# Optimization experiments

Measured on AMD Instinct MI355X. Metric: run time of the kernel, lower is better.

## Reference

```python
import jax, jax.numpy as jnp
import numpy as np

V = 32000  # vocab size
H = 128    # embedding dim
B = 16     # batch
S = 256    # seq len

def setup_inputs() -> dict:
    key = jax.random.key(0)
    k1, k2, k3 = jax.random.split(key, 3)
    src = jax.random.randint(k1, (B, S), 0, V, dtype=jnp.int64)
    W = jax.random.normal(k2, (H, V), dtype=jnp.float32) * 0.02  # nn.Linear(v, h).weight: [h, v]
    b = jax.random.normal(k3, (H,), dtype=jnp.float32) * 0.02    # nn.Linear bias: [h]
    return {"src": src, "W": W, "b": b}

def reference(src, W, b):
    # Original: one-hot(src) [B,S,V] @ W.T [V,H] + b  (disguised embedding gather).
    onehot = jax.nn.one_hot(src, V, dtype=W.dtype)          # [B, S, V]
    out = jnp.einsum('bsv,hv->bsh', onehot, W) + b          # [B, S, H]
    return out
```

## Files before the change

kernel.cpp:

```cpp
#include <hip/hip_runtime.h>
#include <hip/hip_bf16.h>


#define VOCAB  32000
#define HDIM   128
#define NTOK   (16 * 256)
#define VPB    32
#define NBLK   (VOCAB / VPB)
#define STRIDE 33

__global__ __launch_bounds__(256) void embed_scatter_kernel(
    const int* __restrict__ src,
    const float* __restrict__ W,
    const float* __restrict__ bias,
    float* __restrict__ out)
{
    __shared__ float tile[HDIM * STRIDE];
    __shared__ int   list[NTOK];
    __shared__ int   nmatch;

    const int t  = threadIdx.x;
    const int v0 = blockIdx.x * VPB;

    if (t == 0) nmatch = 0;
    __syncthreads();

    {
        const int c4 = t & 7;
        const int h0 = t >> 3;
        for (int h = h0; h < HDIM; h += 32) {
            const float4 v = *(const float4*)(W + (size_t)h * VOCAB + v0 + c4 * 4);
            float* dst = &tile[h * STRIDE + c4 * 4];
            dst[0] = v.x; dst[1] = v.y; dst[2] = v.z; dst[3] = v.w;
        }
    }

    {
        const int4* src4 = (const int4*)src;
        for (int i = t; i < NTOK / 4; i += 256) {
            const int4 s = src4[i];
            const int base = i << 2;
            unsigned d;
            d = (unsigned)(s.x - v0); if (d < VPB) list[atomicAdd(&nmatch, 1)] = ((base + 0) << 5) | (int)d;
            d = (unsigned)(s.y - v0); if (d < VPB) list[atomicAdd(&nmatch, 1)] = ((base + 1) << 5) | (int)d;
            d = (unsigned)(s.z - v0); if (d < VPB) list[atomicAdd(&nmatch, 1)] = ((base + 2) << 5) | (int)d;
            d = (unsigned)(s.w - v0); if (d < VPB) list[atomicAdd(&nmatch, 1)] = ((base + 3) << 5) | (int)d;
        }
    }
    __syncthreads();

    const int    n      = nmatch;
    const int    lane32 = t & 31;
    const int    h0     = lane32 * 4;
    const float4 bb     = ((const float4*)bias)[lane32];
    for (int j = t >> 5; j < n; j += 8) {
        const int e   = list[j];
        const int tok = e >> 5;
        const int col = e & 31;
        float4 r;
        r.x = tile[(h0 + 0) * STRIDE + col] + bb.x;
        r.y = tile[(h0 + 1) * STRIDE + col] + bb.y;
        r.z = tile[(h0 + 2) * STRIDE + col] + bb.z;
        r.w = tile[(h0 + 3) * STRIDE + col] + bb.w;
        *(float4*)(out + (size_t)tok * HDIM + h0) = r;
    }
}

extern "C" void kernel_launch(void* const* d_in, const int* in_sizes, int n_in,
                              void* d_out, int out_size, void* d_ws, size_t ws_size,
                              hipStream_t stream) {
    const int*   src  = (const int*)d_in[0];
    const float* W    = (const float*)d_in[1];
    const float* bias = (const float*)d_in[2];
    float*       out  = (float*)d_out;

    embed_scatter_kernel<<<NBLK, 256, 0, stream>>>(src, W, bias, out);
}
```

Baseline: 9.874 us.

## Replace shared atomics with per-wave ballot compaction and overlap loads

Drops the shared-memory atomicAdd counter used to build the match list. Each 64-lane wave now compacts its matches with ballot/popcount into its own list segment. All src and W loads are issued up front into registers before the shared stores, so global latency overlaps and one barrier is removed. The output phase walks the four per-wave lists with one 64-lane wave per token row writing float2, in place of half-waves writing float4. The cost is more registers per thread and a different store width.

```diff
diff --git a/kernel.cpp b/kernel.cpp
--- a/kernel.cpp
+++ b/kernel.cpp
@@ -17,52 +17,69 @@
 {
     __shared__ float tile[HDIM * STRIDE];
     __shared__ int   list[NTOK];
-    __shared__ int   nmatch;
+    __shared__ int   counts[4];
 
-    const int t  = threadIdx.x;
-    const int v0 = blockIdx.x * VPB;
+    const int t    = threadIdx.x;
+    const int lane = t & 63;
+    const int wav  = t >> 6;
+    const int v0   = blockIdx.x * VPB;
 
-    if (t == 0) nmatch = 0;
+    const int4* src4 = (const int4*)src;
+    int4 sv[4];
+#pragma unroll
+    for (int it = 0; it < 4; ++it) sv[it] = src4[t + (it << 8)];
+
+    const int c4 = t & 7;
+    const int hh = t >> 3;
+    float4 wv[4];
+#pragma unroll
+    for (int k = 0; k < 4; ++k)
+        wv[k] = *(const float4*)(W + (size_t)(hh + (k << 5)) * VOCAB + v0 + (c4 << 2));
+
+    const float2 bb = ((const float2*)bias)[lane];
+
+    int cnt = 0;
+    const unsigned long long ltmask = (1ull << lane) - 1ull;
+    int* mylist = list + (wav << 10);
+#pragma unroll
+    for (int it = 0; it < 4; ++it) {
+        const int base = (t + (it << 8)) << 2;
+        const int vals[4] = {sv[it].x, sv[it].y, sv[it].z, sv[it].w};
+#pragma unroll
+        for (int e = 0; e < 4; ++e) {
+            const unsigned d = (unsigned)(vals[e] - v0);
+            const bool pred = d < VPB;
+            const unsigned long long mask = __ballot(pred);
+            if (mask) {
+                if (pred)
+                    mylist[cnt + (int)__popcll(mask & ltmask)] = ((base + e) << 5) | (int)d;
+                cnt += (int)__popcll(mask);
+            }
+        }
+    }
+    if (lane == 0) counts[wav] = cnt;
+
+#pragma unroll
+    for (int k = 0; k < 4; ++k) {
+        float* dst = &tile[(hh + (k << 5)) * STRIDE + (c4 << 2)];
+        dst[0] = wv[k].x; dst[1] = wv[k].y; dst[2] = wv[k].z; dst[3] = wv[k].w;
+    }
+
     __syncthreads();
 
-    {
-        const int c4 = t & 7;
-        const int h0 = t >> 3;
-        for (int h = h0; h < HDIM; h += 32) {
-            const float4 v = *(const float4*)(W + (size_t)h * VOCAB + v0 + c4 * 4);
-            float* dst = &tile[h * STRIDE + c4 * 4];
-            dst[0] = v.x; dst[1] = v.y; dst[2] = v.z; dst[3] = v.w;
+    const int h0 = lane << 1;
+    for (int w = 0; w < 4; ++w) {
+        const int  n  = counts[w];
+        const int* lw = list + (w << 10);
+        for (int j = wav; j < n; j += 4) {
+            const int e   = lw[j];
+            const int tok = e >> 5;
+            const int col = e & 31;
+            float2 r;
+            r.x = tile[(h0 + 0) * STRIDE + col] + bb.x;
+            r.y = tile[(h0 + 1) * STRIDE + col] + bb.y;
+            *(float2*)(out + (size_t)tok * HDIM + h0) = r;
         }
-    }
-
-    {
-        const int4* src4 = (const int4*)src;
-        for (int i = t; i < NTOK / 4; i += 256) {
-            const int4 s = src4[i];
-            const int base = i << 2;
-            unsigned d;
-            d = (unsigned)(s.x - v0); if (d < VPB) list[atomicAdd(&nmatch, 1)] = ((base + 0) << 5) | (int)d;
-            d = (unsigned)(s.y - v0); if (d < VPB) list[atomicAdd(&nmatch, 1)] = ((base + 1) << 5) | (int)d;
-            d = (unsigned)(s.z - v0); if (d < VPB) list[atomicAdd(&nmatch, 1)] = ((base + 2) << 5) | (int)d;
-            d = (unsigned)(s.w - v0); if (d < VPB) list[atomicAdd(&nmatch, 1)] = ((base + 3) << 5) | (int)d;
-        }
-    }
-    __syncthreads();
-
-    const int    n      = nmatch;
-    const int    lane32 = t & 31;
-    const int    h0     = lane32 * 4;
-    const float4 bb     = ((const float4*)bias)[lane32];
-    for (int j = t >> 5; j < n; j += 8) {
-        const int e   = list[j];
-        const int tok = e >> 5;
-        const int col = e & 31;
-        float4 r;
-        r.x = tile[(h0 + 0) * STRIDE + col] + bb.x;
-        r.y = tile[(h0 + 1) * STRIDE + col] + bb.y;
-        r.z = tile[(h0 + 2) * STRIDE + col] + bb.z;
-        r.w = tile[(h0 + 3) * STRIDE + col] + bb.w;
-        *(float4*)(out + (size_t)tok * HDIM + h0) = r;
     }
 }
 
```

After: 9.863 us. Within noise of the previous version (-0.1%).
